# Optimization experiments

Hardware: AMD Instinct MI355X
Metric: run time of the kernel (lower is better)

The kernel has to match this reference:

```python
import jax, jax.numpy as jnp
import numpy as np

BN_EPS = 1e-5

def setup_inputs() -> dict:
    key = jax.random.key(0)
    ks = jax.random.split(key, 11)
    B, C, H, W = 8, 256, 64, 64
    Ci = 128
    s_in = 1.0 / np.sqrt(C)   # kaiming-uniform-ish scale for 1x1 convs
    s_ci = 1.0 / np.sqrt(Ci)
    return {
        "x": jax.random.normal(ks[0], (B, C, H, W), dtype=jnp.float32),
        "g_w": jax.random.normal(ks[1], (Ci, C), dtype=jnp.float32) * s_in,
        "g_b": jax.random.normal(ks[2], (Ci,), dtype=jnp.float32) * s_in,
        "theta_w": jax.random.normal(ks[3], (Ci, C), dtype=jnp.float32) * s_in,
        "theta_b": jax.random.normal(ks[4], (Ci,), dtype=jnp.float32) * s_in,
        "phi_w": jax.random.normal(ks[5], (Ci, C), dtype=jnp.float32) * s_in,
        "phi_b": jax.random.normal(ks[6], (Ci,), dtype=jnp.float32) * s_in,
        "W_w": jax.random.normal(ks[7], (C, Ci), dtype=jnp.float32) * s_ci,
        "W_b": jax.random.normal(ks[8], (C,), dtype=jnp.float32) * s_ci,
        "bn_gamma": jax.random.uniform(ks[9], (C,), dtype=jnp.float32),
        "bn_beta": jax.random.normal(ks[10], (C,), dtype=jnp.float32) * 0.1,
    }

def _proj(w, b, xf):
    # 1x1 conv as channel GEMM: w [O,C], xf [B,C,N] -> [B,O,N]
    return jnp.einsum('oc,bcn->bon', w, xf) + b[None, :, None]

def reference(x, g_w, g_b, theta_w, theta_b, phi_w, phi_b, W_w, W_b, bn_gamma, bn_beta):
    B, C, H, W = x.shape
    N = H * W
    xf = x.reshape(B, C, N)
    g_x = _proj(g_w, g_b, xf).transpose(0, 2, 1)       # [B,N,Ci]
    theta_x = _proj(theta_w, theta_b, xf).transpose(0, 2, 1)  # [B,N,Ci]
    phi_x = _proj(phi_w, phi_b, xf)                     # [B,Ci,N]
    # unscaled single-head spatial attention
    f = jnp.einsum('bnc,bcm->bnm', theta_x, phi_x)      # [B,N,N]
    f_div_C = jax.nn.softmax(f, axis=-1)
    y = jnp.einsum('bnm,bmc->bnc', f_div_C, g_x)        # [B,N,Ci]
    y = y.transpose(0, 2, 1)                            # [B,Ci,N]
    Wy = _proj(W_w, W_b, y)                             # [B,C,N]
    # BatchNorm2d in training mode: stats over (B, N) per channel (biased var)
    mean = jnp.mean(Wy, axis=(0, 2), keepdims=True)
    var = jnp.mean((Wy - mean) ** 2, axis=(0, 2), keepdims=True)
    Wy_hat = (Wy - mean) * jax.lax.rsqrt(var + BN_EPS)
    Wy_bn = Wy_hat * bn_gamma[None, :, None] + bn_beta[None, :, None]
    z = Wy_bn.reshape(B, C, H, W) + x
    return z
```

## Files before the change

### kernel.cpp

```cpp
#include <hip/hip_runtime.h>
#include <cstddef>

#define NB 8
#define NC 256
#define NN 4096
#define NCI 128

typedef unsigned short ushort_t;
typedef __attribute__((ext_vector_type(8))) short bf16x8;
typedef __attribute__((ext_vector_type(4))) short bf16x4;
typedef __attribute__((ext_vector_type(4))) float f32x4;
typedef __attribute__((ext_vector_type(8))) unsigned short ushort8v;
typedef __attribute__((ext_vector_type(4))) unsigned short ushort4v;

__device__ __forceinline__ ushort_t f2bf(float f) {
  union { float f; unsigned int u; } x; x.f = f;
  unsigned int r = x.u + 0x7FFFu + ((x.u >> 16) & 1u);
  return (ushort_t)(r >> 16);
}
__device__ __forceinline__ float bf2f(ushort_t h) {
  union { unsigned int u; float f; } x; x.u = ((unsigned int)h) << 16;
  return x.f;
}
__device__ __forceinline__ void gld16(const void* g, void* l) {
  __builtin_amdgcn_global_load_lds(
      (const __attribute__((address_space(1))) unsigned int*)g,
      (__attribute__((address_space(3))) unsigned int*)l, 16, 0, 0);
}

__global__ __launch_bounds__(512) void conv_w_kernel(
    const float* __restrict__ th_w, const float* __restrict__ ph_w,
    const float* __restrict__ g_w,  const float* __restrict__ W_w,
    ushort_t* __restrict__ thw, ushort_t* __restrict__ thwl,
    ushort_t* __restrict__ phw, ushort_t* __restrict__ phwl,
    ushort_t* __restrict__ gw,  ushort_t* __restrict__ Wwf)
{
    const int t16 = blockIdx.x;
    const int p   = blockIdx.y;
    const int u = threadIdx.x >> 6, lane = threadIdx.x & 63;
    if (p < 3 && t16 >= 8) return;
    if (p == 3 && u >= 4) return;
    const float* w = (p == 0) ? th_w : (p == 1) ? ph_w : (p == 2) ? g_w : W_w;
    ushort_t* oh  = (p == 0) ? thw  : (p == 1) ? phw  : (p == 2) ? gw  : Wwf;
    ushort_t* ol  = (p == 0) ? thwl : (p == 1) ? phwl : nullptr;
    const int stride = (p == 3) ? NCI : NC;
    const int fr = t16 * 16 + (lane & 15);
    ushort8v hv, lv;
#pragma unroll
    for (int j = 0; j < 8; ++j) {
        int c = 32 * u + 8 * (lane >> 4) + j;
        float v = w[(size_t)fr * stride + c];
        ushort_t hi = f2bf(v);
        hv[j] = hi;
        lv[j] = f2bf(v - bf2f(hi));
    }
    size_t o = (p == 3) ? (((size_t)t16 * 4 + u) * 64 + lane) * 8
                        : (((size_t)t16 * 8 + u) * 64 + lane) * 8;
    *(ushort8v*)(oh + o) = hv;
    if (p < 2) *(ushort8v*)(ol + o) = lv;
}

__global__ __launch_bounds__(256, 2) void proj_mfma_kernel(
    const float* __restrict__ x,
    const ushort_t* __restrict__ thw, const ushort_t* __restrict__ thwl,
    const ushort_t* __restrict__ phw, const ushort_t* __restrict__ phwl,
    const ushort_t* __restrict__ gw,
    const float* __restrict__ th_b, const float* __restrict__ ph_b,
    const float* __restrict__ g_b,
    ushort_t* __restrict__ thh,
    ushort_t* __restrict__ phh, ushort_t* __restrict__ phl,
    ushort_t* __restrict__ gfr)
{
    const int tid = threadIdx.x;
    const int lane = tid & 63, wv = tid >> 6;
    const int b  = blockIdx.x >> 6;
    const int nt = (blockIdx.x & 63) * 4 + wv;
    const int h = lane >> 4, li = lane & 15;

    bf16x8 xh[8], xl[8];
#pragma unroll
    for (int u = 0; u < 8; ++u) {
#pragma unroll
        for (int j = 0; j < 8; ++j) {
            int c = 32 * u + 8 * h + j;
            float v = x[((size_t)b * NC + c) * NN + nt * 16 + li];
            ushort_t hi = f2bf(v);
            xh[u][j] = (short)hi;
            xl[u][j] = (short)f2bf(v - bf2f(hi));
        }
    }

#pragma unroll
    for (int u2 = 0; u2 < 4; ++u2) {
        f32x4 D0 = (f32x4){0.f,0.f,0.f,0.f}, D1 = (f32x4){0.f,0.f,0.f,0.f};
#pragma unroll
        for (int u = 0; u < 8; ++u) {
            bf16x8 a0h = *(const bf16x8*)(thw  + ((size_t)(2*u2)   * 8 + u) * 512 + lane * 8);
            bf16x8 a0l = *(const bf16x8*)(thwl + ((size_t)(2*u2)   * 8 + u) * 512 + lane * 8);
            bf16x8 a1h = *(const bf16x8*)(thw  + ((size_t)(2*u2+1) * 8 + u) * 512 + lane * 8);
            bf16x8 a1l = *(const bf16x8*)(thwl + ((size_t)(2*u2+1) * 8 + u) * 512 + lane * 8);
            D0 = __builtin_amdgcn_mfma_f32_16x16x32_bf16(a0h, xh[u], D0, 0, 0, 0);
            D0 = __builtin_amdgcn_mfma_f32_16x16x32_bf16(a0h, xl[u], D0, 0, 0, 0);
            D0 = __builtin_amdgcn_mfma_f32_16x16x32_bf16(a0l, xh[u], D0, 0, 0, 0);
            D1 = __builtin_amdgcn_mfma_f32_16x16x32_bf16(a1h, xh[u], D1, 0, 0, 0);
            D1 = __builtin_amdgcn_mfma_f32_16x16x32_bf16(a1h, xl[u], D1, 0, 0, 0);
            D1 = __builtin_amdgcn_mfma_f32_16x16x32_bf16(a1l, xh[u], D1, 0, 0, 0);
        }
        ushort8v hv;
#pragma unroll
        for (int r = 0; r < 4; ++r) hv[r]     = f2bf(D0[r] + th_b[u2 * 32 + 4 * h + r]);
#pragma unroll
        for (int r = 0; r < 4; ++r) hv[4 + r] = f2bf(D1[r] + th_b[u2 * 32 + 16 + 4 * h + r]);
        *(ushort8v*)(thh + (((size_t)b * 256 + nt) * 4 + u2) * 512 + lane * 8) = hv;
    }

#pragma unroll
    for (int u2 = 0; u2 < 4; ++u2) {
        f32x4 D0 = (f32x4){0.f,0.f,0.f,0.f}, D1 = (f32x4){0.f,0.f,0.f,0.f};
#pragma unroll
        for (int u = 0; u < 8; ++u) {
            bf16x8 a0h = *(const bf16x8*)(phw  + ((size_t)(2*u2)   * 8 + u) * 512 + lane * 8);
            bf16x8 a0l = *(const bf16x8*)(phwl + ((size_t)(2*u2)   * 8 + u) * 512 + lane * 8);
            bf16x8 a1h = *(const bf16x8*)(phw  + ((size_t)(2*u2+1) * 8 + u) * 512 + lane * 8);
            bf16x8 a1l = *(const bf16x8*)(phwl + ((size_t)(2*u2+1) * 8 + u) * 512 + lane * 8);
            D0 = __builtin_amdgcn_mfma_f32_16x16x32_bf16(a0h, xh[u], D0, 0, 0, 0);
            D0 = __builtin_amdgcn_mfma_f32_16x16x32_bf16(a0h, xl[u], D0, 0, 0, 0);
            D0 = __builtin_amdgcn_mfma_f32_16x16x32_bf16(a0l, xh[u], D0, 0, 0, 0);
            D1 = __builtin_amdgcn_mfma_f32_16x16x32_bf16(a1h, xh[u], D1, 0, 0, 0);
            D1 = __builtin_amdgcn_mfma_f32_16x16x32_bf16(a1h, xl[u], D1, 0, 0, 0);
            D1 = __builtin_amdgcn_mfma_f32_16x16x32_bf16(a1l, xh[u], D1, 0, 0, 0);
        }
        ushort8v hv, lv;
#pragma unroll
        for (int r = 0; r < 4; ++r) {
            float v = D0[r] + ph_b[u2 * 32 + 4 * h + r];
            ushort_t hi = f2bf(v);
            hv[r] = hi; lv[r] = f2bf(v - bf2f(hi));
        }
#pragma unroll
        for (int r = 0; r < 4; ++r) {
            float v = D1[r] + ph_b[u2 * 32 + 16 + 4 * h + r];
            ushort_t hi = f2bf(v);
            hv[4 + r] = hi; lv[4 + r] = f2bf(v - bf2f(hi));
        }
        size_t o = (((size_t)b * 256 + nt) * 4 + u2) * 512 + lane * 8;
        *(ushort8v*)(phh + o) = hv;
        *(ushort8v*)(phl + o) = lv;
    }

#pragma unroll
    for (int cit = 0; cit < 8; ++cit) {
        f32x4 D = (f32x4){0.f,0.f,0.f,0.f};
#pragma unroll
        for (int u = 0; u < 8; ++u) {
            bf16x8 bv = *(const bf16x8*)(gw + ((size_t)cit * 8 + u) * 512 + lane * 8);
            D = __builtin_amdgcn_mfma_f32_16x16x32_bf16(xh[u], bv, D, 0, 0, 0);
        }
        float gb = g_b[cit * 16 + li];
        ushort4v pv;
#pragma unroll
        for (int r = 0; r < 4; ++r) pv[r] = f2bf(D[r] + gb);
        *(ushort4v*)(gfr + (((size_t)b * 256 + nt) * 4 + (cit >> 1)) * 512
                         + lane * 8 + (cit & 1) * 4) = pv;
    }
}

__global__ __launch_bounds__(256, 2) void attn_mfma_kernel(
    const ushort_t* __restrict__ thh,
    const ushort_t* __restrict__ phh, const ushort_t* __restrict__ phl,
    const ushort_t* __restrict__ gfr, float* __restrict__ pacc,
    float* __restrict__ pl)
{
    __shared__ __align__(16) char smem[36864];
    const int tid  = threadIdx.x;
    const int lane = tid & 63;
    const int wv   = tid >> 6;
    const int batch = blockIdx.x & 7;
    const int ih    = blockIdx.x >> 3;
    const int half  = ih & 1;
    const int qblk  = ih >> 1;
    const int qt0   = qblk * 8 + wv * 2;

    bf16x8 qh[2][4];
#pragma unroll
    for (int q = 0; q < 2; ++q)
#pragma unroll
        for (int u = 0; u < 4; ++u)
            qh[q][u] = *(const bf16x8*)(thh + (((size_t)batch * 256 + qt0 + q) * 4 + u) * 512 + (size_t)lane * 8);

    f32x4 accy[2][8];
#pragma unroll
    for (int q = 0; q < 2; ++q)
#pragma unroll
        for (int c = 0; c < 8; ++c) accy[q][c] = (f32x4){0.f, 0.f, 0.f, 0.f};
    float l_run[2] = {0.f, 0.f};

    const ushort_t* Kh = phh + (size_t)batch * 524288 + (size_t)half * 262144;
    const ushort_t* Kl = phl + (size_t)batch * 524288 + (size_t)half * 262144;
    const ushort_t* Vg = gfr + (size_t)batch * 524288 + (size_t)half * 262144;

    {
        size_t off0 = (size_t)tid * 8;
        gld16(Kh + off0, smem + tid * 16);
        gld16(Kl + off0, smem + 4096 + tid * 16);
        gld16(Vg + off0, smem + 8192 + tid * 16);
        size_t off1 = off0 + 2048;
        gld16(Kh + off1, smem + 12288 + tid * 16);
        gld16(Kl + off1, smem + 12288 + 4096 + tid * 16);
        gld16(Vg + off1, smem + 12288 + 8192 + tid * 16);
    }

    int cb = 0;
    for (int t = 0; t < 128; ++t) {
        if (t < 127) { asm volatile("s_waitcnt vmcnt(3)" ::: "memory"); }
        else         { asm volatile("s_waitcnt vmcnt(0)" ::: "memory"); }
        __builtin_amdgcn_s_barrier();
        __builtin_amdgcn_sched_barrier(0);

        if (t < 126) {
            int sb = cb + 2; if (sb >= 3) sb -= 3;
            size_t off = (size_t)(t + 2) * 2048 + (size_t)tid * 8;
            char* bp = smem + sb * 12288;
            gld16(Kh + off, bp + tid * 16);
            gld16(Kl + off, bp + 4096 + tid * 16);
            gld16(Vg + off, bp + 8192 + tid * 16);
        }
        const char* buf = smem + cb * 12288;

        __builtin_amdgcn_s_setprio(1);
        f32x4 sA0 = (f32x4){0.f,0.f,0.f,0.f};
        f32x4 sA1 = (f32x4){0.f,0.f,0.f,0.f};
        f32x4 sB0 = (f32x4){0.f,0.f,0.f,0.f};
        f32x4 sB1 = (f32x4){0.f,0.f,0.f,0.f};
#pragma unroll
        for (int u = 0; u < 4; ++u) {
            bf16x8 kh = *(const bf16x8*)(buf + u * 1024 + lane * 16);
            bf16x8 kl = *(const bf16x8*)(buf + 4096 + u * 1024 + lane * 16);
            sA0 = __builtin_amdgcn_mfma_f32_16x16x32_bf16(kh, qh[0][u], sA0, 0, 0, 0);
            sA1 = __builtin_amdgcn_mfma_f32_16x16x32_bf16(kh, qh[1][u], sA1, 0, 0, 0);
            sB0 = __builtin_amdgcn_mfma_f32_16x16x32_bf16(kl, qh[0][u], sB0, 0, 0, 0);
            sB1 = __builtin_amdgcn_mfma_f32_16x16x32_bf16(kl, qh[1][u], sB1, 0, 0, 0);
        }
        __builtin_amdgcn_s_setprio(0);

        bf16x4 pa[2];
#pragma unroll
        for (int q = 0; q < 2; ++q) {
            f32x4 s = (q == 0) ? (sA0 + sB0) : (sA1 + sB1);
            float p0 = exp2f(fmaf(s[0], 1.4426950408889634f, -86.56170245333781f));
            float p1 = exp2f(fmaf(s[1], 1.4426950408889634f, -86.56170245333781f));
            float p2 = exp2f(fmaf(s[2], 1.4426950408889634f, -86.56170245333781f));
            float p3 = exp2f(fmaf(s[3], 1.4426950408889634f, -86.56170245333781f));
            l_run[q] += (p0 + p1) + (p2 + p3);
            union { unsigned int w[2]; bf16x4 v; } pk;
            union { float f; unsigned int u; } b0, b1, b2, b3;
            b0.f = p0; b1.f = p1; b2.f = p2; b3.f = p3;
            pk.w[0] = (b0.u >> 16) | (b1.u & 0xFFFF0000u);
            pk.w[1] = (b2.u >> 16) | (b3.u & 0xFFFF0000u);
            pa[q] = pk.v;
        }

        __builtin_amdgcn_s_setprio(1);
#pragma unroll
        for (int p = 0; p < 4; ++p) {
            bf16x8 v8 = *(const bf16x8*)(buf + 8192 + p * 1024 + lane * 16);
            bf16x4 v0 = {v8[0], v8[1], v8[2], v8[3]};
            bf16x4 v1 = {v8[4], v8[5], v8[6], v8[7]};
            accy[0][2*p]   = __builtin_amdgcn_mfma_f32_16x16x16bf16_1k(pa[0], v0, accy[0][2*p],   0, 0, 0);
            accy[1][2*p]   = __builtin_amdgcn_mfma_f32_16x16x16bf16_1k(pa[1], v0, accy[1][2*p],   0, 0, 0);
            accy[0][2*p+1] = __builtin_amdgcn_mfma_f32_16x16x16bf16_1k(pa[0], v1, accy[0][2*p+1], 0, 0, 0);
            accy[1][2*p+1] = __builtin_amdgcn_mfma_f32_16x16x16bf16_1k(pa[1], v1, accy[1][2*p+1], 0, 0, 0);
        }
        __builtin_amdgcn_s_setprio(0);
        __builtin_amdgcn_sched_barrier(0);

        cb = cb + 1; if (cb >= 3) cb -= 3;
    }

#pragma unroll
    for (int q = 0; q < 2; ++q) {
        l_run[q] += __shfl_xor(l_run[q], 16);
        l_run[q] += __shfl_xor(l_run[q], 32);
    }

    const int h = lane >> 4, li = lane & 15;
#pragma unroll
    for (int q = 0; q < 2; ++q) {
        float* pp = pacc + (size_t)half * 4194304
                  + ((size_t)batch * NN + (size_t)(qt0 + q) * 16) * NCI + li;
#pragma unroll
        for (int cit = 0; cit < 8; ++cit) {
            pp[(4 * h + 0) * NCI + cit * 16] = accy[q][cit][0];
            pp[(4 * h + 1) * NCI + cit * 16] = accy[q][cit][1];
            pp[(4 * h + 2) * NCI + cit * 16] = accy[q][cit][2];
            pp[(4 * h + 3) * NCI + cit * 16] = accy[q][cit][3];
        }
        if (lane < 16)
            pl[(((size_t)half * 8 + batch) * 256 + qt0 + q) * 16 + lane] = l_run[q];
    }
}

__global__ __launch_bounds__(256) void wy_kernel(
    const float* __restrict__ pacc, const float* __restrict__ pl,
    const ushort_t* __restrict__ Wwf, const float* __restrict__ W_b,
    float* __restrict__ Wy, float* __restrict__ bs, float* __restrict__ bs2)
{
    __shared__ ushort_t ys[8192];
    const int tid = threadIdx.x;
    const int lane = tid & 63, wv = tid >> 6;
    const int b = blockIdx.x >> 6;
    const int n0 = (blockIdx.x & 63) << 6;

    {
        const int nn = tid >> 2;
        const int q4 = tid & 3;
        const int n = n0 + nn;
        const int qt = n >> 4, qq = n & 15;
        float l0 = pl[((size_t)b * 256 + qt) * 16 + qq];
        float l1 = pl[((size_t)(8 + b) * 256 + qt) * 16 + qq];
        float inv = 1.0f / (l0 + l1);
        const float* p0 = pacc + ((size_t)b * NN + n) * NCI + q4 * 32;
        const float* p1 = p0 + 4194304;
#pragma unroll
        for (int gi = 0; gi < 4; ++gi) {
            float4 a0 = *(const float4*)(p0 + gi * 8);
            float4 a1 = *(const float4*)(p0 + gi * 8 + 4);
            float4 c0 = *(const float4*)(p1 + gi * 8);
            float4 c1 = *(const float4*)(p1 + gi * 8 + 4);
            ushort8v v;
            v[0] = f2bf((a0.x + c0.x) * inv);
            v[1] = f2bf((a0.y + c0.y) * inv);
            v[2] = f2bf((a0.z + c0.z) * inv);
            v[3] = f2bf((a0.w + c0.w) * inv);
            v[4] = f2bf((a1.x + c1.x) * inv);
            v[5] = f2bf((a1.y + c1.y) * inv);
            v[6] = f2bf((a1.z + c1.z) * inv);
            v[7] = f2bf((a1.w + c1.w) * inv);
            int sg = (q4 * 4 + gi) ^ (nn & 7);
            *(ushort8v*)(ys + nn * 128 + sg * 8) = v;
        }
    }
    __syncthreads();

    const int h = lane >> 4, li = lane & 15;
    bf16x8 wa[4][4];
#pragma unroll
    for (int ct = 0; ct < 4; ++ct)
#pragma unroll
        for (int kc = 0; kc < 4; ++kc)
            wa[ct][kc] = *(const bf16x8*)(Wwf + (((size_t)(wv * 4 + ct) * 4 + kc) * 64 + lane) * 8);
    float wb[4][4];
#pragma unroll
    for (int ct = 0; ct < 4; ++ct)
#pragma unroll
        for (int r = 0; r < 4; ++r)
            wb[ct][r] = W_b[wv * 64 + ct * 16 + 4 * h + r];

    float ps[4][4], ps2[4][4];
#pragma unroll
    for (int ct = 0; ct < 4; ++ct)
#pragma unroll
        for (int r = 0; r < 4; ++r) { ps[ct][r] = 0.f; ps2[ct][r] = 0.f; }

#pragma unroll
    for (int ct = 0; ct < 4; ++ct)
#pragma unroll
        for (int nt = 0; nt < 4; ++nt) {
            f32x4 D = (f32x4){0.f, 0.f, 0.f, 0.f};
            const int nn = nt * 16 + li;
#pragma unroll
            for (int kc = 0; kc < 4; ++kc) {
                int sg = (4 * kc + h) ^ (nn & 7);
                bf16x8 bv = *(const bf16x8*)(ys + nn * 128 + sg * 8);
                D = __builtin_amdgcn_mfma_f32_16x16x32_bf16(wa[ct][kc], bv, D, 0, 0, 0);
            }
            float* o = Wy + ((size_t)b * NC + wv * 64 + ct * 16 + 4 * h) * NN + n0 + nn;
#pragma unroll
            for (int r = 0; r < 4; ++r) {
                float v = D[r] + wb[ct][r];
                o[(size_t)r * NN] = v;
                ps[ct][r]  += v;
                ps2[ct][r] += v * v;
            }
        }

#pragma unroll
    for (int ct = 0; ct < 4; ++ct)
#pragma unroll
        for (int r = 0; r < 4; ++r) {
#pragma unroll
            for (int off = 1; off <= 8; off <<= 1) {
                ps[ct][r]  += __shfl_xor(ps[ct][r],  off);
                ps2[ct][r] += __shfl_xor(ps2[ct][r], off);
            }
        }
    if (li == 0) {
#pragma unroll
        for (int ct = 0; ct < 4; ++ct)
#pragma unroll
            for (int r = 0; r < 4; ++r) {
                int c = wv * 64 + ct * 16 + 4 * h + r;
                bs [(size_t)c * 512 + blockIdx.x] = ps[ct][r];
                bs2[(size_t)c * 512 + blockIdx.x] = ps2[ct][r];
            }
    }
}

__global__ __launch_bounds__(256) void bn_stats_kernel(
    const float* __restrict__ bs, const float* __restrict__ bs2,
    const float* __restrict__ gamma, const float* __restrict__ beta,
    float* __restrict__ scale, float* __restrict__ shift)
{
    const int c = blockIdx.x;
    const int tid = threadIdx.x;
    float s  = bs [(size_t)c * 512 + tid] + bs [(size_t)c * 512 + tid + 256];
    float s2 = bs2[(size_t)c * 512 + tid] + bs2[(size_t)c * 512 + tid + 256];
#pragma unroll
    for (int off = 1; off < 64; off <<= 1) {
        s  += __shfl_xor(s, off);
        s2 += __shfl_xor(s2, off);
    }
    __shared__ float red[8];
    const int wid = tid >> 6;
    if ((tid & 63) == 0) { red[wid] = s; red[4 + wid] = s2; }
    __syncthreads();
    if (tid == 0) {
        float S  = red[0] + red[1] + red[2] + red[3];
        float S2 = red[4] + red[5] + red[6] + red[7];
        const float invn = 1.f / (float)(NB * NN);
        float mean = S * invn;
        float var  = S2 * invn - mean * mean;
        float rstd = rsqrtf(var + 1e-5f);
        float sc = gamma[c] * rstd;
        scale[c] = sc;
        shift[c] = beta[c] - mean * sc;
    }
}

__global__ __launch_bounds__(256) void bn_apply_kernel(
    const float* __restrict__ Wy, const float* __restrict__ x,
    const float* __restrict__ scale, const float* __restrict__ shift,
    float* __restrict__ out)
{
    const size_t i4 = (size_t)blockIdx.x * 256 + threadIdx.x;
    const int c = (int)((i4 >> 10) & 255);
    float4 w  = ((const float4*)Wy)[i4];
    float4 xv = ((const float4*)x)[i4];
    const float sc = scale[c], sh = shift[c];
    float4 o;
    o.x = w.x * sc + sh + xv.x;
    o.y = w.y * sc + sh + xv.y;
    o.z = w.z * sc + sh + xv.z;
    o.w = w.w * sc + sh + xv.w;
    ((float4*)out)[i4] = o;
}

extern "C" void kernel_launch(void* const* d_in, const int* in_sizes, int n_in,
                              void* d_out, int out_size, void* d_ws, size_t ws_size,
                              hipStream_t stream) {
    const float* x     = (const float*)d_in[0];
    const float* g_w   = (const float*)d_in[1];
    const float* g_b   = (const float*)d_in[2];
    const float* th_w  = (const float*)d_in[3];
    const float* th_b  = (const float*)d_in[4];
    const float* ph_w  = (const float*)d_in[5];
    const float* ph_b  = (const float*)d_in[6];
    const float* W_w   = (const float*)d_in[7];
    const float* W_b   = (const float*)d_in[8];
    const float* gamma = (const float*)d_in[9];
    const float* beta  = (const float*)d_in[10];
    float* out = (float*)d_out;
    float* ws  = (float*)d_ws;

    ushort_t* thh = (ushort_t*)(ws);
    ushort_t* phh = (ushort_t*)(ws + 2097152);
    ushort_t* phl = (ushort_t*)(ws + 4194304);
    ushort_t* gfr = (ushort_t*)(ws + 6291456);
    float* Wy     = ws;
    float* pacc   = ws + 8388608;
    float* pl     = ws + 16777216;
    float* scale  = ws + 16842752;
    float* shift  = ws + 16843008;
    ushort_t* thw  = (ushort_t*)(ws + 16843264);
    ushort_t* phw  = (ushort_t*)(ws + 16859648);
    ushort_t* gw   = (ushort_t*)(ws + 16876032);
    ushort_t* Wwf  = (ushort_t*)(ws + 16892416);
    ushort_t* thwl = (ushort_t*)(ws + 16908800);
    ushort_t* phwl = (ushort_t*)(ws + 16925184);
    float* bs  = ws + 16941568;
    float* bs2 = ws + 17072640;

    conv_w_kernel<<<dim3(16, 4), 512, 0, stream>>>(
        th_w, ph_w, g_w, W_w, thw, thwl, phw, phwl, gw, Wwf);
    proj_mfma_kernel<<<512, 256, 0, stream>>>(
        x, thw, thwl, phw, phwl, gw, th_b, ph_b, g_b, thh, phh, phl, gfr);
    attn_mfma_kernel<<<512, 256, 0, stream>>>(thh, phh, phl, gfr, pacc, pl);
    wy_kernel<<<512, 256, 0, stream>>>(pacc, pl, Wwf, W_b, Wy, bs, bs2);
    bn_stats_kernel<<<256, 256, 0, stream>>>(bs, bs2, gamma, beta, scale, shift);
    bn_apply_kernel<<<8192, 256, 0, stream>>>(Wy, x, scale, shift, out);
}
```

Before: 209.5 us.

## Use 32-key tiles with K=32 MFMA for PV and double-buffered LDS

```diff
diff --git a/kernel.cpp b/kernel.cpp
--- a/kernel.cpp
+++ b/kernel.cpp
@@ -114,6 +114,9 @@
         *(ushort8v*)(thh + (((size_t)b * 256 + nt) * 4 + u2) * 512 + lane * 8) = hv;
     }
 
+    const int m32  = ((nt & 1) << 4) | li;
+    const int mtp  = (m32 >> 2) & 1;
+    const int rowp = ((m32 >> 3) << 2) | (m32 & 3);
 #pragma unroll
     for (int u2 = 0; u2 < 4; ++u2) {
         f32x4 D0 = (f32x4){0.f,0.f,0.f,0.f}, D1 = (f32x4){0.f,0.f,0.f,0.f};
@@ -143,11 +146,14 @@
             ushort_t hi = f2bf(v);
             hv[4 + r] = hi; lv[4 + r] = f2bf(v - bf2f(hi));
         }
-        size_t o = (((size_t)b * 256 + nt) * 4 + u2) * 512 + lane * 8;
+        size_t o = ((((size_t)b * 128 + (nt >> 1)) * 2 + mtp) * 4 + u2) * 512
+                 + (size_t)(rowp + 16 * h) * 8;
         *(ushort8v*)(phh + o) = hv;
         *(ushort8v*)(phl + o) = lv;
     }
 
+    const int h2 = (nt & 1) * 2 + (h >> 1);
+    const int j0 = (h & 1) * 4;
 #pragma unroll
     for (int cit = 0; cit < 8; ++cit) {
         f32x4 D = (f32x4){0.f,0.f,0.f,0.f};
@@ -160,8 +166,9 @@
         ushort4v pv;
 #pragma unroll
         for (int r = 0; r < 4; ++r) pv[r] = f2bf(D[r] + gb);
-        *(ushort4v*)(gfr + (((size_t)b * 256 + nt) * 4 + (cit >> 1)) * 512
-                         + lane * 8 + (cit & 1) * 4) = pv;
+        size_t o = (((size_t)b * 128 + (nt >> 1)) * 8 + cit) * 512
+                 + (size_t)(li + 16 * h2) * 8 + j0;
+        *(ushort4v*)(gfr + o) = pv;
     }
 }
 
@@ -171,7 +178,7 @@
     const ushort_t* __restrict__ gfr, float* __restrict__ pacc,
     float* __restrict__ pl)
 {
-    __shared__ __align__(16) char smem[36864];
+    __shared__ __align__(16) char smem[49152];
     const int tid  = threadIdx.x;
     const int lane = tid & 63;
     const int wv   = tid >> 6;
@@ -200,81 +207,87 @@
     const ushort_t* Vg = gfr + (size_t)batch * 524288 + (size_t)half * 262144;
 
     {
-        size_t off0 = (size_t)tid * 8;
-        gld16(Kh + off0, smem + tid * 16);
-        gld16(Kl + off0, smem + 4096 + tid * 16);
-        gld16(Vg + off0, smem + 8192 + tid * 16);
-        size_t off1 = off0 + 2048;
-        gld16(Kh + off1, smem + 12288 + tid * 16);
-        gld16(Kl + off1, smem + 12288 + 4096 + tid * 16);
-        gld16(Vg + off1, smem + 12288 + 8192 + tid * 16);
-    }
-
-    int cb = 0;
-    for (int t = 0; t < 128; ++t) {
-        if (t < 127) { asm volatile("s_waitcnt vmcnt(3)" ::: "memory"); }
-        else         { asm volatile("s_waitcnt vmcnt(0)" ::: "memory"); }
-        __builtin_amdgcn_s_barrier();
-        __builtin_amdgcn_sched_barrier(0);
-
-        if (t < 126) {
-            int sb = cb + 2; if (sb >= 3) sb -= 3;
-            size_t off = (size_t)(t + 2) * 2048 + (size_t)tid * 8;
-            char* bp = smem + sb * 12288;
-            gld16(Kh + off, bp + tid * 16);
-            gld16(Kl + off, bp + 4096 + tid * 16);
-            gld16(Vg + off, bp + 8192 + tid * 16);
-        }
-        const char* buf = smem + cb * 12288;
+        size_t off = (size_t)tid * 8;
+        gld16(Kh + off,        smem + tid * 16);
+        gld16(Kh + off + 2048, smem + 4096  + tid * 16);
+        gld16(Kl + off,        smem + 8192  + tid * 16);
+        gld16(Kl + off + 2048, smem + 12288 + tid * 16);
+        gld16(Vg + off,        smem + 16384 + tid * 16);
+        gld16(Vg + off + 2048, smem + 20480 + tid * 16);
+    }
+    __syncthreads();
+
+    for (int t = 0; t < 64; ++t) {
+        const int cb = t & 1;
+        if (t < 63) {
+            size_t off = (size_t)(t + 1) * 4096 + (size_t)tid * 8;
+            char* b2 = smem + (cb ^ 1) * 24576;
+            gld16(Kh + off,        b2 + tid * 16);
+            gld16(Kh + off + 2048, b2 + 4096  + tid * 16);
+            gld16(Kl + off,        b2 + 8192  + tid * 16);
+            gld16(Kl + off + 2048, b2 + 12288 + tid * 16);
+            gld16(Vg + off,        b2 + 16384 + tid * 16);
+            gld16(Vg + off + 2048, b2 + 20480 + tid * 16);
+        }
+        const char* buf = smem + cb * 24576;
 
         __builtin_amdgcn_s_setprio(1);
-        f32x4 sA0 = (f32x4){0.f,0.f,0.f,0.f};
-        f32x4 sA1 = (f32x4){0.f,0.f,0.f,0.f};
-        f32x4 sB0 = (f32x4){0.f,0.f,0.f,0.f};
-        f32x4 sB1 = (f32x4){0.f,0.f,0.f,0.f};
+        f32x4 sA[2][2], sB[2][2];
+#pragma unroll
+        for (int q = 0; q < 2; ++q)
+#pragma unroll
+            for (int mt = 0; mt < 2; ++mt) {
+                sA[q][mt] = (f32x4){0.f,0.f,0.f,0.f};
+                sB[q][mt] = (f32x4){0.f,0.f,0.f,0.f};
+            }
 #pragma unroll
         for (int u = 0; u < 4; ++u) {
-            bf16x8 kh = *(const bf16x8*)(buf + u * 1024 + lane * 16);
-            bf16x8 kl = *(const bf16x8*)(buf + 4096 + u * 1024 + lane * 16);
-            sA0 = __builtin_amdgcn_mfma_f32_16x16x32_bf16(kh, qh[0][u], sA0, 0, 0, 0);
-            sA1 = __builtin_amdgcn_mfma_f32_16x16x32_bf16(kh, qh[1][u], sA1, 0, 0, 0);
-            sB0 = __builtin_amdgcn_mfma_f32_16x16x32_bf16(kl, qh[0][u], sB0, 0, 0, 0);
-            sB1 = __builtin_amdgcn_mfma_f32_16x16x32_bf16(kl, qh[1][u], sB1, 0, 0, 0);
+            bf16x8 kh0 = *(const bf16x8*)(buf + (0 * 4 + u) * 1024 + lane * 16);
+            bf16x8 kh1 = *(const bf16x8*)(buf + (1 * 4 + u) * 1024 + lane * 16);
+            bf16x8 kl0 = *(const bf16x8*)(buf + 8192 + (0 * 4 + u) * 1024 + lane * 16);
+            bf16x8 kl1 = *(const bf16x8*)(buf + 8192 + (1 * 4 + u) * 1024 + lane * 16);
+            sA[0][0] = __builtin_amdgcn_mfma_f32_16x16x32_bf16(kh0, qh[0][u], sA[0][0], 0, 0, 0);
+            sA[1][0] = __builtin_amdgcn_mfma_f32_16x16x32_bf16(kh0, qh[1][u], sA[1][0], 0, 0, 0);
+            sA[0][1] = __builtin_amdgcn_mfma_f32_16x16x32_bf16(kh1, qh[0][u], sA[0][1], 0, 0, 0);
+            sA[1][1] = __builtin_amdgcn_mfma_f32_16x16x32_bf16(kh1, qh[1][u], sA[1][1], 0, 0, 0);
+            sB[0][0] = __builtin_amdgcn_mfma_f32_16x16x32_bf16(kl0, qh[0][u], sB[0][0], 0, 0, 0);
+            sB[1][0] = __builtin_amdgcn_mfma_f32_16x16x32_bf16(kl0, qh[1][u], sB[1][0], 0, 0, 0);
+            sB[0][1] = __builtin_amdgcn_mfma_f32_16x16x32_bf16(kl1, qh[0][u], sB[0][1], 0, 0, 0);
+            sB[1][1] = __builtin_amdgcn_mfma_f32_16x16x32_bf16(kl1, qh[1][u], sB[1][1], 0, 0, 0);
         }
         __builtin_amdgcn_s_setprio(0);
 
-        bf16x4 pa[2];
+        bf16x8 pa[2];
 #pragma unroll
         for (int q = 0; q < 2; ++q) {
-            f32x4 s = (q == 0) ? (sA0 + sB0) : (sA1 + sB1);
-            float p0 = exp2f(fmaf(s[0], 1.4426950408889634f, -86.56170245333781f));
-            float p1 = exp2f(fmaf(s[1], 1.4426950408889634f, -86.56170245333781f));
-            float p2 = exp2f(fmaf(s[2], 1.4426950408889634f, -86.56170245333781f));
-            float p3 = exp2f(fmaf(s[3], 1.4426950408889634f, -86.56170245333781f));
-            l_run[q] += (p0 + p1) + (p2 + p3);
-            union { unsigned int w[2]; bf16x4 v; } pk;
-            union { float f; unsigned int u; } b0, b1, b2, b3;
-            b0.f = p0; b1.f = p1; b2.f = p2; b3.f = p3;
-            pk.w[0] = (b0.u >> 16) | (b1.u & 0xFFFF0000u);
-            pk.w[1] = (b2.u >> 16) | (b3.u & 0xFFFF0000u);
+            union { unsigned int w[4]; bf16x8 v; } pk;
+            float lsum = 0.f;
+#pragma unroll
+            for (int mt = 0; mt < 2; ++mt) {
+                f32x4 s = sA[q][mt] + sB[q][mt];
+                float p0 = exp2f(fmaf(s[0], 1.4426950408889634f, -86.56170245333781f));
+                float p1 = exp2f(fmaf(s[1], 1.4426950408889634f, -86.56170245333781f));
+                float p2 = exp2f(fmaf(s[2], 1.4426950408889634f, -86.56170245333781f));
+                float p3 = exp2f(fmaf(s[3], 1.4426950408889634f, -86.56170245333781f));
+                lsum += (p0 + p1) + (p2 + p3);
+                union { float f; unsigned int u; } b0, b1, b2, b3;
+                b0.f = p0; b1.f = p1; b2.f = p2; b3.f = p3;
+                pk.w[2 * mt]     = (b0.u >> 16) | (b1.u & 0xFFFF0000u);
+                pk.w[2 * mt + 1] = (b2.u >> 16) | (b3.u & 0xFFFF0000u);
+            }
+            l_run[q] += lsum;
             pa[q] = pk.v;
         }
 
         __builtin_amdgcn_s_setprio(1);
 #pragma unroll
-        for (int p = 0; p < 4; ++p) {
-            bf16x8 v8 = *(const bf16x8*)(buf + 8192 + p * 1024 + lane * 16);
-            bf16x4 v0 = {v8[0], v8[1], v8[2], v8[3]};
-            bf16x4 v1 = {v8[4], v8[5], v8[6], v8[7]};
-            accy[0][2*p]   = __builtin_amdgcn_mfma_f32_16x16x16bf16_1k(pa[0], v0, accy[0][2*p],   0, 0, 0);
-            accy[1][2*p]   = __builtin_amdgcn_mfma_f32_16x16x16bf16_1k(pa[1], v0, accy[1][2*p],   0, 0, 0);
-            accy[0][2*p+1] = __builtin_amdgcn_mfma_f32_16x16x16bf16_1k(pa[0], v1, accy[0][2*p+1], 0, 0, 0);
-            accy[1][2*p+1] = __builtin_amdgcn_mfma_f32_16x16x16bf16_1k(pa[1], v1, accy[1][2*p+1], 0, 0, 0);
+        for (int cit = 0; cit < 8; ++cit) {
+            bf16x8 vf = *(const bf16x8*)(buf + 16384 + cit * 1024 + lane * 16);
+            accy[0][cit] = __builtin_amdgcn_mfma_f32_16x16x32_bf16(pa[0], vf, accy[0][cit], 0, 0, 0);
+            accy[1][cit] = __builtin_amdgcn_mfma_f32_16x16x32_bf16(pa[1], vf, accy[1][cit], 0, 0, 0);
         }
         __builtin_amdgcn_s_setprio(0);
-        __builtin_amdgcn_sched_barrier(0);
-
-        cb = cb + 1; if (cb >= 3) cb -= 3;
+        __syncthreads();
     }
 
 #pragma unroll
```

Result: faster. 201.2 us (-4.0%).
